# Kernel tuning notes

Hardware: AMD Instinct MI355X
Metric: run time of the kernel (lower is better)

## Reference

```python
import jax, jax.numpy as jnp
import numpy as np

KERNEL_SIZE = 2  # matches init kernel_size
EPS = 1e-6


def setup_inputs() -> dict:
    key = jax.random.key(0)
    x = jax.random.uniform(key, (8, 64, 256, 256), dtype=jnp.float32)
    return {"x": x}


def reference(x) -> jnp.ndarray:
    k = KERNEL_SIZE
    b, c, h, w = x.shape
    hp, wp = h - k + 1, w - k + 1  # stride-1 unfold output dims
    n = k * k
    # Gather the k*k shifted views (equivalent to unfold(2,k,1).unfold(3,k,1)).
    # Fixed small loop over k*k offsets, not over data dims.
    windows = jnp.stack(
        [x[:, :, i:i + hp, j:j + wp] for i in range(k) for j in range(k)],
        axis=-1,
    )  # (b, c, hp, wp, n)
    windows = windows.reshape(b, c, hp * wp, n)
    p = windows / (jnp.sum(windows, axis=-1, keepdims=True) + EPS)
    ent = -jnp.sum(p * jnp.log(p + EPS), axis=-1)  # (b, c, hp*wp)
    return ent
```

## Files before the change

### kernel.cpp

```cpp
#include <hip/hip_runtime.h>

#define H    256
#define W    256
#define HP   255
#define WP   255
#define PIX  (HP * WP)
#define NBC  512
#define EPS  1e-6f
#define LN2  0.69314718055994531f

#define GROUPS_PER_IMG (HP * 64)

__global__ __launch_bounds__(256) void entropy_k2_kernel(
    const float* __restrict__ x, float* __restrict__ out)
{
    const int bc = blockIdx.y;
    const int t  = blockIdx.x * 256 + threadIdx.x;
    if (t >= GROUPS_PER_IMG) return;

    const int i  = t >> 6;
    const int j0 = (t & 63) << 2;

    const float* img = x + (size_t)bc * (H * W);
    const float* r0  = img + i * W + j0;
    const float* r1  = r0 + W;

    const float4 a4 = *(const float4*)r0;
    const float4 b4 = *(const float4*)r1;
    const int j4 = (j0 + 4 < W) ? 4 : 3;
    const float a5 = r0[j4];
    const float b5 = r1[j4];

    const float a[5] = {a4.x, a4.y, a4.z, a4.w, a5};
    const float b[5] = {b4.x, b4.y, b4.z, b4.w, b5};

    float res[4];
#pragma unroll
    for (int m = 0; m < 4; ++m) {
        const float w0 = a[m], w1 = a[m + 1];
        const float w2 = b[m], w3 = b[m + 1];
        const float s    = w0 + w1 + w2 + w3 + EPS;
        const float rinv = __builtin_amdgcn_rcpf(s);
        const float p0 = w0 * rinv;
        const float p1 = w1 * rinv;
        const float p2 = w2 * rinv;
        const float p3 = w3 * rinv;
        const float acc = p0 * __builtin_amdgcn_logf(p0 + EPS)
                        + p1 * __builtin_amdgcn_logf(p1 + EPS)
                        + p2 * __builtin_amdgcn_logf(p2 + EPS)
                        + p3 * __builtin_amdgcn_logf(p3 + EPS);
        res[m] = -LN2 * acc;
    }

    float* o = out + (size_t)bc * PIX + i * WP + j0;
#pragma unroll
    for (int m = 0; m < 4; ++m)
        if (j0 + m < WP) o[m] = res[m];
}

extern "C" void kernel_launch(void* const* d_in, const int* in_sizes, int n_in,
                              void* d_out, int out_size, void* d_ws, size_t ws_size,
                              hipStream_t stream)
{
    const float* x   = (const float*)d_in[0];
    float*       out = (float*)d_out;

    dim3 grid((GROUPS_PER_IMG + 255) / 256, NBC);
    entropy_k2_kernel<<<grid, 256, 0, stream>>>(x, out);
}
```

Baseline: 237.1 us.

## Rewrite entropy as S·logS minus sliding sum of w·logw, reuse rows

Result: slower. 247.3 us (+4.3%).

```diff
diff --git a/kernel.cpp b/kernel.cpp
--- a/kernel.cpp
+++ b/kernel.cpp
@@ -9,53 +9,81 @@
 #define EPS  1e-6f
 #define LN2  0.69314718055994531f
 
-#define GROUPS_PER_IMG (HP * 64)
+#define ROWS 17
+#define RG   15
+#define TPI  (RG * 64)
+#define NBLK (TPI * NBC / 256)
+
+typedef float f4 __attribute__((ext_vector_type(4)));
+typedef f4 uf4 __attribute__((aligned(4)));
 
 __global__ __launch_bounds__(256) void entropy_k2_kernel(
     const float* __restrict__ x, float* __restrict__ out)
 {
-    const int bc = blockIdx.y;
     const int t  = blockIdx.x * 256 + threadIdx.x;
-    if (t >= GROUPS_PER_IMG) return;
+    const int bc = t / TPI;
+    const int r  = t - bc * TPI;
+    const int i0 = (r >> 6) * ROWS;
+    const int j0 = (r & 63) << 2;
 
-    const int i  = t >> 6;
-    const int j0 = (t & 63) << 2;
+    const float* img   = x   + (size_t)bc * (H * W);
+    float*       obase = out + (size_t)bc * PIX + j0;
 
-    const float* img = x + (size_t)bc * (H * W);
-    const float* r0  = img + i * W + j0;
-    const float* r1  = r0 + W;
+    const int j4 = (j0 + 4 < W) ? 4 : 3;
+    const bool full = (j0 != 252);
 
-    const float4 a4 = *(const float4*)r0;
-    const float4 b4 = *(const float4*)r1;
-    const int j4 = (j0 + 4 < W) ? 4 : 3;
-    const float a5 = r0[j4];
-    const float b5 = r1[j4];
+    float phw0, phw1, phw2, phw3;
+    float pht0, pht1, pht2, pht3;
 
-    const float a[5] = {a4.x, a4.y, a4.z, a4.w, a5};
-    const float b[5] = {b4.x, b4.y, b4.z, b4.w, b5};
+#pragma unroll 2
+    for (int rr = 0; rr <= ROWS; ++rr) {
+        const int i = i0 + rr;
+        const float* row = img + i * W + j0;
+        const f4    v  = *(const f4*)row;
+        const float a4 = row[j4];
 
-    float res[4];
-#pragma unroll
-    for (int m = 0; m < 4; ++m) {
-        const float w0 = a[m], w1 = a[m + 1];
-        const float w2 = b[m], w3 = b[m + 1];
-        const float s    = w0 + w1 + w2 + w3 + EPS;
-        const float rinv = __builtin_amdgcn_rcpf(s);
-        const float p0 = w0 * rinv;
-        const float p1 = w1 * rinv;
-        const float p2 = w2 * rinv;
-        const float p3 = w3 * rinv;
-        const float acc = p0 * __builtin_amdgcn_logf(p0 + EPS)
-                        + p1 * __builtin_amdgcn_logf(p1 + EPS)
-                        + p2 * __builtin_amdgcn_logf(p2 + EPS)
-                        + p3 * __builtin_amdgcn_logf(p3 + EPS);
-        res[m] = -LN2 * acc;
+        const float a0 = v.x, a1 = v.y, a2 = v.z, a3 = v.w;
+        const float l0 = a0 * __builtin_amdgcn_logf(a0 + EPS);
+        const float l1 = a1 * __builtin_amdgcn_logf(a1 + EPS);
+        const float l2 = a2 * __builtin_amdgcn_logf(a2 + EPS);
+        const float l3 = a3 * __builtin_amdgcn_logf(a3 + EPS);
+        const float l4 = a4 * __builtin_amdgcn_logf(a4 + EPS);
+
+        const float hw0 = a0 + a1, hw1 = a1 + a2, hw2 = a2 + a3, hw3 = a3 + a4;
+        const float ht0 = l0 + l1, ht1 = l1 + l2, ht2 = l2 + l3, ht3 = l3 + l4;
+
+        if (rr > 0) {
+            f4 e;
+            {
+                const float Wm = phw0 + hw0, Tm = pht0 + ht0;
+                const float s = Wm + EPS, rs = __builtin_amdgcn_rcpf(s);
+                e.x = LN2 * (Wm * __builtin_amdgcn_logf(s) - Tm) * rs;
+            }
+            {
+                const float Wm = phw1 + hw1, Tm = pht1 + ht1;
+                const float s = Wm + EPS, rs = __builtin_amdgcn_rcpf(s);
+                e.y = LN2 * (Wm * __builtin_amdgcn_logf(s) - Tm) * rs;
+            }
+            {
+                const float Wm = phw2 + hw2, Tm = pht2 + ht2;
+                const float s = Wm + EPS, rs = __builtin_amdgcn_rcpf(s);
+                e.z = LN2 * (Wm * __builtin_amdgcn_logf(s) - Tm) * rs;
+            }
+            {
+                const float Wm = phw3 + hw3, Tm = pht3 + ht3;
+                const float s = Wm + EPS, rs = __builtin_amdgcn_rcpf(s);
+                e.w = LN2 * (Wm * __builtin_amdgcn_logf(s) - Tm) * rs;
+            }
+            float* o = obase + (size_t)(i - 1) * WP;
+            if (full) {
+                *(uf4*)o = e;
+            } else {
+                o[0] = e.x; o[1] = e.y; o[2] = e.z;
+            }
+        }
+        phw0 = hw0; phw1 = hw1; phw2 = hw2; phw3 = hw3;
+        pht0 = ht0; pht1 = ht1; pht2 = ht2; pht3 = ht3;
     }
-
-    float* o = out + (size_t)bc * PIX + i * WP + j0;
-#pragma unroll
-    for (int m = 0; m < 4; ++m)
-        if (j0 + m < WP) o[m] = res[m];
 }
 
 extern "C" void kernel_launch(void* const* d_in, const int* in_sizes, int n_in,
@@ -64,7 +92,5 @@
 {
     const float* x   = (const float*)d_in[0];
     float*       out = (float*)d_out;
-
-    dim3 grid((GROUPS_PER_IMG + 255) / 256, NBC);
-    entropy_k2_kernel<<<grid, 256, 0, stream>>>(x, out);
+    entropy_k2_kernel<<<dim3(NBLK), 256, 0, stream>>>(x, out);
 }
```

## Rewrite entropy via per-element w·log w and reuse across two output rows

Applied to the files above, without the earlier changes.

Measured after the change: 227.5 us. -4.0%, faster.

```diff
diff --git a/kernel.cpp b/kernel.cpp
--- a/kernel.cpp
+++ b/kernel.cpp
@@ -9,53 +9,93 @@
 #define EPS  1e-6f
 #define LN2  0.69314718055994531f
 
-#define GROUPS_PER_IMG (HP * 64)
+#define TPI   8192
+#define NBLK  (NBC * TPI / 256)
+
+typedef float f4 __attribute__((ext_vector_type(4)));
+
+__device__ __forceinline__ float wlog(float w) {
+    return w * __builtin_amdgcn_logf(w + EPS);
+}
+
+__device__ __forceinline__ float ent4(float Wm, float Tm) {
+    const float s = Wm + EPS;
+    return LN2 * (Wm * __builtin_amdgcn_logf(s) - Tm) * __builtin_amdgcn_rcpf(s);
+}
 
 __global__ __launch_bounds__(256) void entropy_k2_kernel(
     const float* __restrict__ x, float* __restrict__ out)
 {
-    const int bc = blockIdx.y;
     const int t  = blockIdx.x * 256 + threadIdx.x;
-    if (t >= GROUPS_PER_IMG) return;
-
-    const int i  = t >> 6;
-    const int j0 = (t & 63) << 2;
+    const int bc = t >> 13;
+    const int r  = t & (TPI - 1);
+    const int q  = r >> 6;
+    const int j0 = (r & 63) << 2;
+    const int i0 = q << 1;
 
     const float* img = x + (size_t)bc * (H * W);
-    const float* r0  = img + i * W + j0;
-    const float* r1  = r0 + W;
+    const float* r0p = img + i0 * W + j0;
+    const float* r1p = r0p + W;
+    const float* r2p = (q == 127) ? r1p : r1p + W;
+    const int j4 = (j0 + 4 < W) ? 4 : 3;
 
-    const float4 a4 = *(const float4*)r0;
-    const float4 b4 = *(const float4*)r1;
-    const int j4 = (j0 + 4 < W) ? 4 : 3;
-    const float a5 = r0[j4];
-    const float b5 = r1[j4];
+    const f4    va = *(const f4*)r0p;
+    const f4    vb = *(const f4*)r1p;
+    const f4    vc = *(const f4*)r2p;
+    const float a4 = r0p[j4];
+    const float b4 = r1p[j4];
+    const float c4 = r2p[j4];
 
-    const float a[5] = {a4.x, a4.y, a4.z, a4.w, a5};
-    const float b[5] = {b4.x, b4.y, b4.z, b4.w, b5};
+    const float la0 = wlog(va.x), la1 = wlog(va.y), la2 = wlog(va.z),
+                la3 = wlog(va.w), la4 = wlog(a4);
+    const float lb0 = wlog(vb.x), lb1 = wlog(vb.y), lb2 = wlog(vb.z),
+                lb3 = wlog(vb.w), lb4 = wlog(b4);
+    const float lc0 = wlog(vc.x), lc1 = wlog(vc.y), lc2 = wlog(vc.z),
+                lc3 = wlog(vc.w), lc4 = wlog(c4);
 
-    float res[4];
-#pragma unroll
-    for (int m = 0; m < 4; ++m) {
-        const float w0 = a[m], w1 = a[m + 1];
-        const float w2 = b[m], w3 = b[m + 1];
-        const float s    = w0 + w1 + w2 + w3 + EPS;
-        const float rinv = __builtin_amdgcn_rcpf(s);
-        const float p0 = w0 * rinv;
-        const float p1 = w1 * rinv;
-        const float p2 = w2 * rinv;
-        const float p3 = w3 * rinv;
-        const float acc = p0 * __builtin_amdgcn_logf(p0 + EPS)
-                        + p1 * __builtin_amdgcn_logf(p1 + EPS)
-                        + p2 * __builtin_amdgcn_logf(p2 + EPS)
-                        + p3 * __builtin_amdgcn_logf(p3 + EPS);
-        res[m] = -LN2 * acc;
+    const float hwa0 = va.x + va.y, hwa1 = va.y + va.z, hwa2 = va.z + va.w, hwa3 = va.w + a4;
+    const float hwb0 = vb.x + vb.y, hwb1 = vb.y + vb.z, hwb2 = vb.z + vb.w, hwb3 = vb.w + b4;
+    const float hwc0 = vc.x + vc.y, hwc1 = vc.y + vc.z, hwc2 = vc.z + vc.w, hwc3 = vc.w + c4;
+    const float hta0 = la0 + la1, hta1 = la1 + la2, hta2 = la2 + la3, hta3 = la3 + la4;
+    const float htb0 = lb0 + lb1, htb1 = lb1 + lb2, htb2 = lb2 + lb3, htb3 = lb3 + lb4;
+    const float htc0 = lc0 + lc1, htc1 = lc1 + lc2, htc2 = lc2 + lc3, htc3 = lc3 + lc4;
+
+    f4 e0, e1;
+    e0.x = ent4(hwa0 + hwb0, hta0 + htb0);
+    e0.y = ent4(hwa1 + hwb1, hta1 + htb1);
+    e0.z = ent4(hwa2 + hwb2, hta2 + htb2);
+    e0.w = ent4(hwa3 + hwb3, hta3 + htb3);
+    e1.x = ent4(hwb0 + hwc0, htb0 + htc0);
+    e1.y = ent4(hwb1 + hwc1, htb1 + htc1);
+    e1.z = ent4(hwb2 + hwc2, htb2 + htc2);
+    e1.w = ent4(hwb3 + hwc3, htb3 + htc3);
+
+    float* o0 = out + (size_t)bc * PIX + i0 * WP + j0;
+    float* o1 = o0 + WP;
+    const bool full = (j0 != 252);
+    const bool row2 = (q != 127);
+
+    if (full) {
+        __builtin_nontemporal_store(e0.x, o0 + 0);
+        __builtin_nontemporal_store(e0.y, o0 + 1);
+        __builtin_nontemporal_store(e0.z, o0 + 2);
+        __builtin_nontemporal_store(e0.w, o0 + 3);
+        if (row2) {
+            __builtin_nontemporal_store(e1.x, o1 + 0);
+            __builtin_nontemporal_store(e1.y, o1 + 1);
+            __builtin_nontemporal_store(e1.z, o1 + 2);
+            __builtin_nontemporal_store(e1.w, o1 + 3);
+        }
+    } else {
+        __builtin_nontemporal_store(e0.x, o0 + 0);
+        __builtin_nontemporal_store(e0.y, o0 + 1);
+        __builtin_nontemporal_store(e0.z, o0 + 2);
+        if (row2) {
+            __builtin_nontemporal_store(e1.x, o1 + 0);
+            __builtin_nontemporal_store(e1.y, o1 + 1);
+            __builtin_nontemporal_store(e1.z, o1 + 2);
+        }
     }
-
-    float* o = out + (size_t)bc * PIX + i * WP + j0;
-#pragma unroll
-    for (int m = 0; m < 4; ++m)
-        if (j0 + m < WP) o[m] = res[m];
 }
 
 extern "C" void kernel_launch(void* const* d_in, const int* in_sizes, int n_in,
@@ -64,7 +104,5 @@
 {
     const float* x   = (const float*)d_in[0];
     float*       out = (float*)d_out;
-
-    dim3 grid((GROUPS_PER_IMG + 255) / 256, NBC);
-    entropy_k2_kernel<<<grid, 256, 0, stream>>>(x, out);
+    entropy_k2_kernel<<<dim3(NBLK), 256, 0, stream>>>(x, out);
 }
```
